# Optimization experiments

Hardware: AMD Instinct MI355X
Metric: run time of the kernel (lower is better)

The kernel has to match this reference:

```python
import math
import jax, jax.numpy as jnp
import numpy as np

HID = 8
QNUM = 22
NUM_A = 11
NUM_LAYER = 6


def _ln(x, g, b, eps=1e-5):
    m = jnp.mean(x, axis=-1, keepdims=True)
    v = jnp.mean((x - m) ** 2, axis=-1, keepdims=True)
    return (x - m) / jnp.sqrt(v + eps) * g + b


def _conv1d_s2(x, w):
    # x: [N, C, L], w: [O, I, K=2], stride 2, no padding, no bias
    return jax.lax.conv_general_dilated(x, w, (2,), 'VALID', dimension_numbers=('NCH', 'OIH', 'NCH'))


def _qembed(hf):
    # product state amplitudes of RY(hf_q)|0> per qubit: [cos(t/2), sin(t/2)], kron over qubits
    c = jnp.cos(hf / 2.0)
    s = jnp.sin(hf / 2.0)
    state = jnp.ones((1,), dtype=hf.dtype)
    for q in range(hf.shape[0]):
        state = jnp.kron(state, jnp.stack([c[q], s[q]]))
    return state  # [2^Q]


def setup_inputs() -> dict:
    key = jax.random.key(0)
    ks = jax.random.split(key, 32)
    ix_list = [2] * NUM_A  # 2 electrons per atom -> n_e = 22 (even, <= QNUM)
    pos_ix = np.concatenate([np.arange(n) for n in ix_list])
    atom_ix = np.concatenate([np.full(n, i) for i, n in enumerate(ix_list)])
    L = NUM_LAYER
    g = lambda i, shp, s=1.0: jax.random.normal(ks[i], shp, dtype=jnp.float32) * s
    return dict(
        pos_a=g(0, (NUM_A, 3), 3.0),
        ix_a=jnp.asarray(ix_list, dtype=jnp.int32),
        pos_ix=jnp.asarray(pos_ix, dtype=jnp.int32),
        atom_ix=jnp.asarray(atom_ix, dtype=jnp.int32),
        rpos_w=g(1, (10, 3), 1.0),
        emb_w=g(2, (HID, 4), 0.5),
        emb_b=jnp.zeros((HID,), jnp.float32),
        Wq=g(3, (L, HID, HID), 0.35), bq=jnp.zeros((L, HID), jnp.float32),
        Wk=g(4, (L, HID, HID), 0.35), bk=jnp.zeros((L, HID), jnp.float32),
        Wv=g(5, (L, HID, HID), 0.35), bv=jnp.zeros((L, HID), jnp.float32),
        Wo=g(6, (L, HID, HID), 0.35), bo=jnp.zeros((L, HID), jnp.float32),
        W1=g(7, (L, 4 * HID, HID), 0.35), b1=jnp.zeros((L, 4 * HID), jnp.float32),
        W2=g(8, (L, HID, 4 * HID), 0.18), b2=jnp.zeros((L, HID), jnp.float32),
        ln1_g=jnp.ones((L, HID), jnp.float32), ln1_b=jnp.zeros((L, HID), jnp.float32),
        ln2_g=jnp.ones((L, HID), jnp.float32), ln2_b=jnp.zeros((L, HID), jnp.float32),
        Wi=g(9, (2 * HID, HID), 0.35), bi=jnp.zeros((2 * HID,), jnp.float32),
        ni_g=jnp.ones((2 * HID,), jnp.float32), ni_b=jnp.zeros((2 * HID,), jnp.float32),
        conv_a_w=g(10, (2 * HID, 2 * HID, 2), 0.25),
        conv_e_w=g(11, (2 * HID, 2 * HID, 2), 0.25),
        Wout=g(12, (2 ** QNUM, 2 * HID), 0.05),
        bout=jnp.zeros((2 ** QNUM,), jnp.float32),
    )


def reference(pos_a, ix_a, pos_ix, atom_ix, rpos_w, emb_w, emb_b,
              Wq, bq, Wk, bk, Wv, bv, Wo, bo, W1, b1, W2, b2,
              ln1_g, ln1_b, ln2_g, ln2_b,
              Wi, bi, ni_g, ni_b, conv_a_w, conv_e_w, Wout, bout):
    n_e = pos_ix.shape[0]
    pos_e = rpos_w[pos_ix] + pos_a[atom_ix]                 # [n_e, 3]
    ae = pos_e[:, None, :] - pos_a[None, :, :]              # [n_e, A, 3]
    r_ae = jnp.linalg.norm(ae, axis=2, keepdims=True)       # [n_e, A, 1]
    seq = jnp.concatenate([ae, r_ae], axis=-1) @ emb_w.T + emb_b  # [n_e, A, HID]
    amp_proto = ix_a.astype(seq.dtype)[None, :, None]       # broadcast of expanded ix_a
    amp_ae = jnp.std(r_ae, ddof=1)
    bias_ae = jnp.mean(r_ae)
    scale = jnp.sqrt(jnp.asarray(HID, seq.dtype))
    for l in range(Wq.shape[0]):
        x = amp_proto * seq
        q = x @ Wq[l].T + bq[l]
        k = x @ Wk[l].T + bk[l]
        v = x @ Wv[l].T + bv[l]
        att = jax.nn.softmax(jnp.einsum('bqh,bkh->bqk', q, k) / scale, axis=-1)
        a = jnp.einsum('bqk,bkh->bqh', att, v) @ Wo[l].T + bo[l]
        x = _ln(x + a, ln1_g[l], ln1_b[l])
        f = jax.nn.relu(x @ W1[l].T + b1[l]) @ W2[l].T + b2[l]
        seq = _ln(x + f, ln2_g[l], ln2_b[l])
    # pseudo-inverse projection (detached in torch)
    ae_inv = jax.lax.stop_gradient(jnp.linalg.inv(emb_w.T @ emb_w) @ emb_w.T)  # [4, HID]
    r = jnp.einsum('h,bah->ba', ae_inv[-1], seq)[..., None]  # [n_e, A, 1]
    r = amp_ae * (r - jnp.mean(r)) / jnp.std(r, ddof=1) + bias_ae
    x = (jnp.exp(-r) * amp_proto * seq) @ Wi.T + bi          # [n_e, A, 2*HID]
    x = jnp.swapaxes(x, -2, -1)                              # [n_e, 2*HID, A]
    y = jnp.mean(x, axis=-1)                                 # [n_e, 2*HID]
    amp_r = jnp.mean(jnp.exp(-jnp.swapaxes(r, -2, -1)), axis=-1)  # [n_e, 1]
    pad = jnp.zeros((x.shape[0], x.shape[1], 1), x.dtype)
    n_iter_a = (x.shape[-1] + 1) // 2
    for _ in range(n_iter_a):
        x = _conv1d_s2(jnp.concatenate([x, pad], axis=-1), conv_a_w)
    x = (amp_r * _ln(y + x[..., 0], ni_g, ni_b)).T           # [2*HID, n_e]
    y = jnp.mean(x, axis=-1)                                 # [2*HID]
    amp_r2 = jnp.mean(amp_r.T, axis=-1)                      # [1]
    x = x[None]                                              # [1, 2*HID, n_e]
    pad = jnp.zeros((1, x.shape[1], 1), x.dtype)
    n_iter_e = (x.shape[-1] + 1) // 2
    for _ in range(n_iter_e):
        x = _conv1d_s2(jnp.concatenate([x, pad], axis=-1), conv_e_w)
    x = amp_r2 * _ln(y + x[0, :, 0], ni_g, ni_b)             # [2*HID]
    psi = x @ Wout.T + bout                                  # [2^QNUM]
    hf = jnp.asarray(([math.pi, 0.0] * (n_e // 2)) + [0.0] * (QNUM - n_e), dtype=psi.dtype)
    bos = _qembed(hf)
    return psi + bos * (2.0 ** (QNUM / 2))
```

## Files before the change

kernel.cpp:

```cpp
#include <hip/hip_runtime.h>
#include <math.h>

#define NE 22
#define NA 11
#define HD 8
#define H2 16
#define QN 22
#define NL 6
#define CPAD 12
#define CSTR 17

struct QCS { float c[QN]; float s[QN]; };

#define RL(v, l) __uint_as_float(__builtin_amdgcn_readlane(__float_as_uint(v), (l)))

__device__ __forceinline__ float block_reduce_sum(float v, float* red, int tid) {
  red[tid] = v;
  __syncthreads();
  for (int off = 128; off > 0; off >>= 1) {
    if (tid < off) red[tid] += red[tid + off];
    __syncthreads();
  }
  float s = red[0];
  __syncthreads();
  return s;
}

__device__ __forceinline__ void ln_vec(const float* x, int n, const float* __restrict__ g,
                                       const float* __restrict__ bb, float* o) {
  float m = 0.f;
  for (int i = 0; i < n; i++) m += x[i];
  m /= (float)n;
  float v = 0.f;
  for (int i = 0; i < n; i++) { float d = x[i] - m; v += d * d; }
  v /= (float)n;
  float is = 1.0f / sqrtf(v + 1e-5f);
  for (int i = 0; i < n; i++) o[i] = (x[i] - m) * is * g[i] + bb[i];
}

__global__ __launch_bounds__(256) void small_net_kernel(
    const float* __restrict__ pos_a, const int* __restrict__ ix_a,
    const int* __restrict__ pos_ix, const int* __restrict__ atom_ix,
    const float* __restrict__ rpos_w, const float* __restrict__ emb_w,
    const float* __restrict__ emb_b,
    const float* __restrict__ Wq, const float* __restrict__ bq,
    const float* __restrict__ Wk, const float* __restrict__ bk,
    const float* __restrict__ Wv, const float* __restrict__ bv,
    const float* __restrict__ Wo, const float* __restrict__ bo,
    const float* __restrict__ W1, const float* __restrict__ b1,
    const float* __restrict__ W2, const float* __restrict__ b2,
    const float* __restrict__ ln1_g, const float* __restrict__ ln1_b,
    const float* __restrict__ ln2_g, const float* __restrict__ ln2_b,
    const float* __restrict__ Wi, const float* __restrict__ bi,
    const float* __restrict__ ni_g, const float* __restrict__ ni_b,
    const float* __restrict__ conv_a_w, const float* __restrict__ conv_e_w,
    float* __restrict__ xf_out)
{
  const int tid = threadIdx.x;
  const int lane = tid & 63;
  const int b = tid / NA;
  const int a = tid % NA;
  const bool act = (tid < NE * NA);

  __shared__ __align__(16) float s_seq[NE][NA][HD];
  __shared__ __align__(16) float s_k[NE][NA][HD];
  __shared__ __align__(16) float s_v[NE][NA][HD];
  __shared__ float s_pos_e[NE][3];
  __shared__ float s_amp[NA];
  __shared__ float s_er[NE][NA];
  __shared__ float s_red[256];
  __shared__ float s_scal[8];
  __shared__ float s_aeinv[HD];
  __shared__ float convA[NE * CPAD * CSTR];
  __shared__ float convB[NE * CPAD * CSTR];
  __shared__ float s_y[NE][H2];
  __shared__ float s_ampr[NE];
  __shared__ float s_eA[24 * CSTR];
  __shared__ float s_eB[24 * CSTR];
  __shared__ float s_y2[H2];
  __shared__ float s_cewt[32 * H2];

  float cwr[8], wir[2];
  #pragma unroll
  for (int j = 0; j < 8; j++) cwr[j] = conv_a_w[j * 64 + lane];
  #pragma unroll
  for (int j = 0; j < 2; j++) wir[j] = Wi[j * 64 + lane];

  for (int s = tid; s < 512; s += 256) {
    int o = s >> 5, i = (s >> 1) & 15, k = s & 1;
    s_cewt[(i * 2 + k) * 16 + o] = conv_e_w[s];
  }

  if (tid < NE) {
    int p = pos_ix[tid], am = atom_ix[tid];
    for (int j = 0; j < 3; j++) s_pos_e[tid][j] = rpos_w[p * 3 + j] + pos_a[am * 3 + j];
  }
  if (tid < NA) s_amp[tid] = (float)ix_a[tid];
  __syncthreads();

  float rae = 0.f;
  if (act) {
    float d0 = s_pos_e[b][0] - pos_a[a * 3 + 0];
    float d1 = s_pos_e[b][1] - pos_a[a * 3 + 1];
    float d2 = s_pos_e[b][2] - pos_a[a * 3 + 2];
    rae = sqrtf(d0 * d0 + d1 * d1 + d2 * d2);
    float in4[4] = { d0, d1, d2, rae };
    #pragma unroll
    for (int h = 0; h < HD; h++) {
      float s = emb_b[h];
      #pragma unroll
      for (int j = 0; j < 4; j++) s += in4[j] * emb_w[h * 4 + j];
      s_seq[b][a][h] = s;
    }
  }
  {
    float sum = block_reduce_sum(act ? rae : 0.f, s_red, tid);
    float mean = sum / (float)(NE * NA);
    float d = act ? (rae - mean) : 0.f;
    float ss = block_reduce_sum(d * d, s_red, tid);
    if (tid == 0) { s_scal[0] = sqrtf(ss / (float)(NE * NA - 1)); s_scal[1] = mean; }
  }
  __syncthreads();

  const float iscale = 0.35355339059327373f;
  for (int l = 0; l < NL; l++) {
    float wr[12];
    wr[0] = Wq[l * 64 + lane];
    wr[1] = Wk[l * 64 + lane];
    wr[2] = Wv[l * 64 + lane];
    wr[3] = Wo[l * 64 + lane];
    #pragma unroll
    for (int j = 0; j < 4; j++) wr[4 + j] = W1[l * 256 + j * 64 + lane];
    #pragma unroll
    for (int j = 0; j < 4; j++) wr[8 + j] = W2[l * 256 + j * 64 + lane];

    float xv[HD], qq[HD];
    if (act) {
      float amp = s_amp[a];
      float4 sq0 = *(const float4*)&s_seq[b][a][0];
      float4 sq1 = *(const float4*)&s_seq[b][a][4];
      xv[0] = amp * sq0.x; xv[1] = amp * sq0.y; xv[2] = amp * sq0.z; xv[3] = amp * sq0.w;
      xv[4] = amp * sq1.x; xv[5] = amp * sq1.y; xv[6] = amp * sq1.z; xv[7] = amp * sq1.w;
      float kk[HD], vv[HD];
      #pragma unroll
      for (int h = 0; h < HD; h++) {
        float q_ = bq[l * HD + h], k_ = bk[l * HD + h], v_ = bv[l * HD + h];
        #pragma unroll
        for (int h2 = 0; h2 < HD; h2++) {
          q_ += xv[h2] * RL(wr[0], h * 8 + h2);
          k_ += xv[h2] * RL(wr[1], h * 8 + h2);
          v_ += xv[h2] * RL(wr[2], h * 8 + h2);
        }
        qq[h] = q_; kk[h] = k_; vv[h] = v_;
      }
      *(float4*)&s_k[b][a][0] = make_float4(kk[0], kk[1], kk[2], kk[3]);
      *(float4*)&s_k[b][a][4] = make_float4(kk[4], kk[5], kk[6], kk[7]);
      *(float4*)&s_v[b][a][0] = make_float4(vv[0], vv[1], vv[2], vv[3]);
      *(float4*)&s_v[b][a][4] = make_float4(vv[4], vv[5], vv[6], vv[7]);
    }
    __syncthreads();
    if (act) {
      float sc[NA];
      float mx = -1e30f;
      #pragma unroll
      for (int ka = 0; ka < NA; ka++) {
        float4 k0 = *(const float4*)&s_k[b][ka][0];
        float4 k1 = *(const float4*)&s_k[b][ka][4];
        float s = qq[0]*k0.x + qq[1]*k0.y + qq[2]*k0.z + qq[3]*k0.w
                + qq[4]*k1.x + qq[5]*k1.y + qq[6]*k1.z + qq[7]*k1.w;
        s *= iscale;
        sc[ka] = s;
        mx = fmaxf(mx, s);
      }
      float den = 0.f;
      #pragma unroll
      for (int ka = 0; ka < NA; ka++) { sc[ka] = expf(sc[ka] - mx); den += sc[ka]; }
      float inv_den = 1.0f / den;
      float av[HD];
      #pragma unroll
      for (int h = 0; h < HD; h++) av[h] = 0.f;
      #pragma unroll
      for (int ka = 0; ka < NA; ka++) {
        float4 v0 = *(const float4*)&s_v[b][ka][0];
        float4 v1 = *(const float4*)&s_v[b][ka][4];
        float p = sc[ka];
        av[0] += p * v0.x; av[1] += p * v0.y; av[2] += p * v0.z; av[3] += p * v0.w;
        av[4] += p * v1.x; av[5] += p * v1.y; av[6] += p * v1.z; av[7] += p * v1.w;
      }
      #pragma unroll
      for (int h = 0; h < HD; h++) av[h] *= inv_den;
      float xr[HD], xn[HD];
      #pragma unroll
      for (int h = 0; h < HD; h++) {
        float t = bo[l * HD + h];
        #pragma unroll
        for (int h2 = 0; h2 < HD; h2++) t += av[h2] * RL(wr[3], h * 8 + h2);
        xr[h] = xv[h] + t;
      }
      ln_vec(xr, HD, ln1_g + l * HD, ln1_b + l * HD, xn);
      float f2[HD];
      #pragma unroll
      for (int h = 0; h < HD; h++) f2[h] = b2[l * HD + h];
      #pragma unroll
      for (int o = 0; o < 32; o++) {
        float t = b1[l * 32 + o];
        #pragma unroll
        for (int h = 0; h < HD; h++) t += xn[h] * RL(wr[4 + ((o * 8 + h) >> 6)], (o * 8 + h) & 63);
        t = fmaxf(t, 0.f);
        #pragma unroll
        for (int h = 0; h < HD; h++) f2[h] += t * RL(wr[8 + ((h * 32 + o) >> 6)], (h * 32 + o) & 63);
      }
      #pragma unroll
      for (int h = 0; h < HD; h++) xr[h] = xn[h] + f2[h];
      ln_vec(xr, HD, ln2_g + l * HD, ln2_b + l * HD, xn);
      *(float4*)&s_seq[b][a][0] = make_float4(xn[0], xn[1], xn[2], xn[3]);
      *(float4*)&s_seq[b][a][4] = make_float4(xn[4], xn[5], xn[6], xn[7]);
    }
    __syncthreads();
  }

  if (tid == 0) {
    double M[4][8];
    for (int i = 0; i < 4; i++)
      for (int j = 0; j < 4; j++) {
        double s = 0.0;
        for (int h = 0; h < HD; h++) s += (double)emb_w[h * 4 + i] * (double)emb_w[h * 4 + j];
        M[i][j] = s;
        M[i][4 + j] = (i == j) ? 1.0 : 0.0;
      }
    for (int c = 0; c < 4; c++) {
      int piv = c;
      for (int r2 = c + 1; r2 < 4; r2++) if (fabs(M[r2][c]) > fabs(M[piv][c])) piv = r2;
      if (piv != c) for (int j = 0; j < 8; j++) { double t = M[c][j]; M[c][j] = M[piv][j]; M[piv][j] = t; }
      double dd = M[c][c];
      for (int j = 0; j < 8; j++) M[c][j] /= dd;
      for (int r2 = 0; r2 < 4; r2++) if (r2 != c) {
        double f = M[r2][c];
        for (int j = 0; j < 8; j++) M[r2][j] -= f * M[c][j];
      }
    }
    for (int h = 0; h < HD; h++) {
      double s = 0.0;
      for (int j = 0; j < 4; j++) s += M[3][4 + j] * (double)emb_w[h * 4 + j];
      s_aeinv[h] = (float)s;
    }
  }
  __syncthreads();

  float rv = 0.f;
  if (act) {
    #pragma unroll
    for (int h = 0; h < HD; h++) rv += s_aeinv[h] * s_seq[b][a][h];
  }
  {
    float sum = block_reduce_sum(act ? rv : 0.f, s_red, tid);
    float rm = sum / (float)(NE * NA);
    float d = act ? (rv - rm) : 0.f;
    float ss = block_reduce_sum(d * d, s_red, tid);
    float rs = sqrtf(ss / (float)(NE * NA - 1));
    if (act) {
      float rr = s_scal[0] * (rv - rm) / rs + s_scal[1];
      s_er[b][a] = expf(-rr);
    }
  }
  __syncthreads();

  if (act) {
    float e2 = s_er[b][a] * s_amp[a];
    float4 sq0 = *(const float4*)&s_seq[b][a][0];
    float4 sq1 = *(const float4*)&s_seq[b][a][4];
    float tv[HD] = { e2*sq0.x, e2*sq0.y, e2*sq0.z, e2*sq0.w,
                     e2*sq1.x, e2*sq1.y, e2*sq1.z, e2*sq1.w };
    #pragma unroll
    for (int o = 0; o < H2; o++) {
      float s = bi[o];
      #pragma unroll
      for (int h = 0; h < HD; h++) s += tv[h] * RL(wir[(o * 8 + h) >> 6], (o * 8 + h) & 63);
      convA[(b * CPAD + a) * CSTR + o] = s;
    }
  }
  for (int z = tid; z < NE * H2; z += 256)
    convA[((z >> 4) * CPAD + 11) * CSTR + (z & 15)] = 0.f;
  __syncthreads();

  for (int idx = tid; idx < NE * H2; idx += 256) {
    int bb = idx >> 4, o = idx & 15;
    float s = 0.f;
    for (int a2 = 0; a2 < NA; a2++) s += convA[(bb * CPAD + a2) * CSTR + o];
    s_y[bb][o] = s / (float)NA;
  }
  if (tid < NE) {
    float s = 0.f;
    for (int a2 = 0; a2 < NA; a2++) s += s_er[tid][a2];
    s_ampr[tid] = s / (float)NA;
  }
  __syncthreads();

  float* pin = convA;
  float* pout = convB;
  int L = NA;
  for (int it = 0; it < 6; it++) {
    int Lo = (L - 1) / 2 + 1;
    for (int pos = tid; pos < NE * Lo; pos += 256) {
      int bb = pos / Lo, j = pos - bb * Lo;
      const float* r0 = pin + (bb * CPAD + 2 * j) * CSTR;
      const float* r1 = r0 + CSTR;
      float x0[16], x1[16];
      #pragma unroll
      for (int i = 0; i < 16; i++) { x0[i] = r0[i]; x1[i] = r1[i]; }
      float* wrow = pout + (bb * CPAD + j) * CSTR;
      #pragma unroll
      for (int o = 0; o < 16; o++) {
        float acc = 0.f;
        #pragma unroll
        for (int i = 0; i < 16; i++) {
          acc += x0[i] * RL(cwr[((o * 16 + i) * 2) >> 6], ((o * 16 + i) * 2) & 63)
               + x1[i] * RL(cwr[((o * 16 + i) * 2 + 1) >> 6], ((o * 16 + i) * 2 + 1) & 63);
        }
        wrow[o] = acc;
      }
    }
    for (int z = tid; z < NE * H2; z += 256)
      pout[((z >> 4) * CPAD + Lo) * CSTR + (z & 15)] = 0.f;
    __syncthreads();
    float* t = pin; pin = pout; pout = t;
    L = Lo;
  }

  if (tid < NE) {
    float t[H2], oo[H2];
    #pragma unroll
    for (int o = 0; o < H2; o++) t[o] = s_y[tid][o] + pin[(tid * CPAD) * CSTR + o];
    ln_vec(t, H2, ni_g, ni_b, oo);
    float ar = s_ampr[tid];
    #pragma unroll
    for (int o = 0; o < H2; o++) s_eA[tid * CSTR + o] = ar * oo[o];
  }
  if (tid < H2) s_eA[NE * CSTR + tid] = 0.f;
  __syncthreads();
  if (tid < H2) {
    float s = 0.f;
    for (int bb = 0; bb < NE; bb++) s += s_eA[bb * CSTR + tid];
    s_y2[tid] = s / (float)NE;
  }
  if (tid == 0) {
    float s = 0.f;
    for (int bb = 0; bb < NE; bb++) s += s_ampr[bb];
    s_scal[4] = s / (float)NE;
  }
  __syncthreads();

  float* pinE = s_eA;
  float* poutE = s_eB;
  L = NE;
  for (int it = 0; it < 11; it++) {
    int Lo = (L - 1) / 2 + 1;
    for (int idx = tid; idx < Lo * H2; idx += 256) {
      int j = idx >> 4, o = idx & 15;
      const float* r0 = pinE + (2 * j) * CSTR;
      const float* r1 = r0 + CSTR;
      float acc = 0.f;
      #pragma unroll
      for (int i = 0; i < 16; i++)
        acc += r0[i] * s_cewt[(i * 2) * 16 + o] + r1[i] * s_cewt[(i * 2 + 1) * 16 + o];
      poutE[j * CSTR + o] = acc;
    }
    if (tid < H2) poutE[Lo * CSTR + tid] = 0.f;
    __syncthreads();
    float* t = pinE; pinE = poutE; poutE = t;
    L = Lo;
  }

  if (tid == 0) {
    float t[H2], oo[H2];
    for (int o = 0; o < H2; o++) t[o] = s_y2[o] + pinE[o];
    ln_vec(t, H2, ni_g, ni_b, oo);
    float a2 = s_scal[4];
    for (int o = 0; o < H2; o++) xf_out[o] = a2 * oo[o];
  }
}

__global__ __launch_bounds__(256) void psi_kernel(
    const float* __restrict__ Wout, const float* __restrict__ bout,
    const float* __restrict__ xf, float* __restrict__ out, QCS cs, int n)
{
  __shared__ float s_xf[H2];
  if (threadIdx.x < H2) s_xf[threadIdx.x] = xf[threadIdx.x];
  __syncthreads();
  int lane = threadIdx.x & 63;
  int waveBase = blockIdx.x * 256 + (threadIdx.x & ~63);
  if (waveBase >= n) return;
  const float4* W4 = (const float4*)Wout + (size_t)waveBase * 4;
  int q = lane & 3;
  float4 xq = make_float4(s_xf[q * 4], s_xf[q * 4 + 1], s_xf[q * 4 + 2], s_xf[q * 4 + 3]);
  #pragma unroll
  for (int j = 0; j < 4; j++) {
    float4 w = W4[j * 64 + lane];
    float p = w.x * xq.x + w.y * xq.y + w.z * xq.z + w.w * xq.w;
    p += __shfl_xor(p, 1, 64);
    p += __shfl_xor(p, 2, 64);
    if (q == 0) {
      int row = waveBase + j * 16 + (lane >> 2);
      float acc = bout[row] + p;
      unsigned int ii = (unsigned int)row;
      float pr = (float)(1 << (QN / 2));
      #pragma unroll
      for (int qb = 0; qb < QN; qb++)
        pr *= ((ii >> (QN - 1 - qb)) & 1u) ? cs.s[qb] : cs.c[qb];
      out[row] = acc + pr;
    }
  }
}

extern "C" void kernel_launch(void* const* d_in, const int* in_sizes, int n_in,
                              void* d_out, int out_size, void* d_ws, size_t ws_size,
                              hipStream_t stream) {
  const float* pos_a   = (const float*)d_in[0];
  const int*   ix_a    = (const int*)d_in[1];
  const int*   pos_ix  = (const int*)d_in[2];
  const int*   atom_ix = (const int*)d_in[3];
  const float* rpos_w  = (const float*)d_in[4];
  const float* emb_w   = (const float*)d_in[5];
  const float* emb_b   = (const float*)d_in[6];
  const float* Wq = (const float*)d_in[7];   const float* bq = (const float*)d_in[8];
  const float* Wk = (const float*)d_in[9];   const float* bk = (const float*)d_in[10];
  const float* Wv = (const float*)d_in[11];  const float* bv = (const float*)d_in[12];
  const float* Wo = (const float*)d_in[13];  const float* bo = (const float*)d_in[14];
  const float* W1 = (const float*)d_in[15];  const float* b1 = (const float*)d_in[16];
  const float* W2 = (const float*)d_in[17];  const float* b2 = (const float*)d_in[18];
  const float* ln1_g = (const float*)d_in[19]; const float* ln1_b = (const float*)d_in[20];
  const float* ln2_g = (const float*)d_in[21]; const float* ln2_b = (const float*)d_in[22];
  const float* Wi = (const float*)d_in[23];  const float* bi = (const float*)d_in[24];
  const float* ni_g = (const float*)d_in[25]; const float* ni_b = (const float*)d_in[26];
  const float* conv_a_w = (const float*)d_in[27];
  const float* conv_e_w = (const float*)d_in[28];
  const float* Wout = (const float*)d_in[29];
  const float* bout = (const float*)d_in[30];
  float* xf = (float*)d_ws;

  small_net_kernel<<<1, 256, 0, stream>>>(pos_a, ix_a, pos_ix, atom_ix, rpos_w,
      emb_w, emb_b, Wq, bq, Wk, bk, Wv, bv, Wo, bo, W1, b1, W2, b2,
      ln1_g, ln1_b, ln2_g, ln2_b, Wi, bi, ni_g, ni_b, conv_a_w, conv_e_w, xf);

  QCS cs;
  int n_e = in_sizes[2];
  for (int q = 0; q < QN; q++) {
    float hf = (q < n_e && (q % 2 == 0)) ? (float)M_PI : 0.0f;
    cs.c[q] = cosf(0.5f * hf);
    cs.s[q] = sinf(0.5f * hf);
  }

  int n = out_size;
  int blocks = (n + 255) / 256;
  psi_kernel<<<blocks, 256, 0, stream>>>(Wout, bout, xf, (float*)d_out, cs, n);
}
```

Before: 504.3 us.

## Split transformer layers into per-electron multi-block kernel before single-block tail

Moves the six attention/MLP layers out of the single 256-thread block into a separate kernel with one 128-thread block per electron. Within each block a thread computes one (atom, hidden) element, and the block exchanges data through shared memory. Sequence and distance results go to workspace for a separate tail kernel that does the reductions and convolutions. The aim is to cut the serial per-thread work on the long single-block critical path by spreading it across many CUs. The cost is an extra kernel launch, a global-memory round trip, and many more block barriers per layer.

```diff
diff --git a/kernel.cpp b/kernel.cpp
--- a/kernel.cpp
+++ b/kernel.cpp
@@ -38,7 +38,7 @@
   for (int i = 0; i < n; i++) o[i] = (x[i] - m) * is * g[i] + bb[i];
 }
 
-__global__ __launch_bounds__(256) void small_net_kernel(
+__global__ __launch_bounds__(128, 1) void layers_kernel(
     const float* __restrict__ pos_a, const int* __restrict__ ix_a,
     const int* __restrict__ pos_ix, const int* __restrict__ atom_ix,
     const float* __restrict__ rpos_w, const float* __restrict__ emb_w,
@@ -51,9 +51,210 @@
     const float* __restrict__ W2, const float* __restrict__ b2,
     const float* __restrict__ ln1_g, const float* __restrict__ ln1_b,
     const float* __restrict__ ln2_g, const float* __restrict__ ln2_b,
+    float* __restrict__ seq_out, float* __restrict__ rae_out)
+{
+  const int e = blockIdx.x;
+  const int tid = threadIdx.x;
+  const int a = tid >> 3;
+  const int h = tid & 7;
+  const bool act = (a < NA);
+
+  __shared__ __align__(16) float sseq[NA][HD];
+  __shared__ __align__(16) float sx[NA][HD];
+  __shared__ __align__(16) float sq_[NA][HD];
+  __shared__ __align__(16) float sk_[NA][HD];
+  __shared__ __align__(16) float sv_[NA][HD];
+  __shared__ __align__(16) float sav[NA][HD];
+  __shared__ float ss[NA][12];
+  __shared__ __align__(16) float sh_[NA][32];
+
+  float amp_a = 0.f;
+  if (act) {
+    amp_a = (float)ix_a[a];
+    int p = pos_ix[e], am = atom_ix[e];
+    float d0 = rpos_w[p*3+0] + pos_a[am*3+0] - pos_a[a*3+0];
+    float d1 = rpos_w[p*3+1] + pos_a[am*3+1] - pos_a[a*3+1];
+    float d2 = rpos_w[p*3+2] + pos_a[am*3+2] - pos_a[a*3+2];
+    float rae = sqrtf(d0*d0 + d1*d1 + d2*d2);
+    float s = emb_b[h] + d0*emb_w[h*4+0] + d1*emb_w[h*4+1]
+            + d2*emb_w[h*4+2] + rae*emb_w[h*4+3];
+    sseq[a][h] = s;
+    if (h == 0) rae_out[e*NA + a] = rae;
+  }
+  __syncthreads();
+
+  const float iscale = 0.35355339059327373f;
+  for (int l = 0; l < NL; l++) {
+    float wq[8], wk[8], wv[8], wo[8], w1v[4][8], w2v[32];
+    {
+      const float4* q4 = (const float4*)(Wq + l*64 + h*8);
+      float4 t0 = q4[0], t1 = q4[1];
+      wq[0]=t0.x; wq[1]=t0.y; wq[2]=t0.z; wq[3]=t0.w; wq[4]=t1.x; wq[5]=t1.y; wq[6]=t1.z; wq[7]=t1.w;
+      const float4* k4 = (const float4*)(Wk + l*64 + h*8);
+      t0 = k4[0]; t1 = k4[1];
+      wk[0]=t0.x; wk[1]=t0.y; wk[2]=t0.z; wk[3]=t0.w; wk[4]=t1.x; wk[5]=t1.y; wk[6]=t1.z; wk[7]=t1.w;
+      const float4* v4 = (const float4*)(Wv + l*64 + h*8);
+      t0 = v4[0]; t1 = v4[1];
+      wv[0]=t0.x; wv[1]=t0.y; wv[2]=t0.z; wv[3]=t0.w; wv[4]=t1.x; wv[5]=t1.y; wv[6]=t1.z; wv[7]=t1.w;
+      const float4* o4 = (const float4*)(Wo + l*64 + h*8);
+      t0 = o4[0]; t1 = o4[1];
+      wo[0]=t0.x; wo[1]=t0.y; wo[2]=t0.z; wo[3]=t0.w; wo[4]=t1.x; wo[5]=t1.y; wo[6]=t1.z; wo[7]=t1.w;
+      #pragma unroll
+      for (int j = 0; j < 4; j++) {
+        const float4* w14 = (const float4*)(W1 + l*256 + (j*8 + h)*8);
+        float4 u0 = w14[0], u1 = w14[1];
+        w1v[j][0]=u0.x; w1v[j][1]=u0.y; w1v[j][2]=u0.z; w1v[j][3]=u0.w;
+        w1v[j][4]=u1.x; w1v[j][5]=u1.y; w1v[j][6]=u1.z; w1v[j][7]=u1.w;
+      }
+      const float4* w24 = (const float4*)(W2 + l*256 + h*32);
+      #pragma unroll
+      for (int j = 0; j < 8; j++) {
+        float4 u = w24[j];
+        w2v[j*4+0]=u.x; w2v[j*4+1]=u.y; w2v[j*4+2]=u.z; w2v[j*4+3]=u.w;
+      }
+    }
+    float bqv = bq[l*8+h], bkv = bk[l*8+h], bvv = bv[l*8+h], bov = bo[l*8+h];
+    float b1v[4];
+    #pragma unroll
+    for (int j = 0; j < 4; j++) b1v[j] = b1[l*32 + j*8 + h];
+    float b2v = b2[l*8+h];
+    float g1 = ln1_g[l*8+h], be1 = ln1_b[l*8+h];
+    float g2 = ln2_g[l*8+h], be2 = ln2_b[l*8+h];
+
+    float xah = 0.f;
+    if (act) { xah = amp_a * sseq[a][h]; sx[a][h] = xah; }
+    __syncthreads();
+
+    if (act) {
+      float xr[8];
+      float4 r0 = *(const float4*)&sx[a][0];
+      float4 r1 = *(const float4*)&sx[a][4];
+      xr[0]=r0.x; xr[1]=r0.y; xr[2]=r0.z; xr[3]=r0.w; xr[4]=r1.x; xr[5]=r1.y; xr[6]=r1.z; xr[7]=r1.w;
+      float q_ = bqv, k_ = bkv, v_ = bvv;
+      #pragma unroll
+      for (int h2 = 0; h2 < 8; h2++) {
+        q_ += xr[h2]*wq[h2];
+        k_ += xr[h2]*wk[h2];
+        v_ += xr[h2]*wv[h2];
+      }
+      sq_[a][h] = q_; sk_[a][h] = k_; sv_[a][h] = v_;
+    }
+    __syncthreads();
+
+    if (act) {
+      float4 q0 = *(const float4*)&sq_[a][0];
+      float4 q1 = *(const float4*)&sq_[a][4];
+      {
+        int ka = h;
+        float4 k0 = *(const float4*)&sk_[ka][0];
+        float4 k1 = *(const float4*)&sk_[ka][4];
+        ss[a][ka] = iscale * (q0.x*k0.x + q0.y*k0.y + q0.z*k0.z + q0.w*k0.w
+                            + q1.x*k1.x + q1.y*k1.y + q1.z*k1.z + q1.w*k1.w);
+      }
+      if (h < 3) {
+        int ka = 8 + h;
+        float4 k0 = *(const float4*)&sk_[ka][0];
+        float4 k1 = *(const float4*)&sk_[ka][4];
+        ss[a][ka] = iscale * (q0.x*k0.x + q0.y*k0.y + q0.z*k0.z + q0.w*k0.w
+                            + q1.x*k1.x + q1.y*k1.y + q1.z*k1.z + q1.w*k1.w);
+      }
+    }
+    __syncthreads();
+
+    float avh = 0.f;
+    if (act) {
+      float sc[NA], mx = -1e30f;
+      #pragma unroll
+      for (int ka = 0; ka < NA; ka++) { sc[ka] = ss[a][ka]; mx = fmaxf(mx, sc[ka]); }
+      float den = 0.f;
+      #pragma unroll
+      for (int ka = 0; ka < NA; ka++) { sc[ka] = expf(sc[ka] - mx); den += sc[ka]; }
+      float inv_den = 1.0f / den;
+      #pragma unroll
+      for (int ka = 0; ka < NA; ka++) avh += sc[ka] * sv_[ka][h];
+      avh *= inv_den;
+      sav[a][h] = avh;
+    }
+    __syncthreads();
+
+    if (act) {
+      float av[8];
+      float4 r0 = *(const float4*)&sav[a][0];
+      float4 r1 = *(const float4*)&sav[a][4];
+      av[0]=r0.x; av[1]=r0.y; av[2]=r0.z; av[3]=r0.w; av[4]=r1.x; av[5]=r1.y; av[6]=r1.z; av[7]=r1.w;
+      float t = bov;
+      #pragma unroll
+      for (int h2 = 0; h2 < 8; h2++) t += av[h2]*wo[h2];
+      sq_[a][h] = xah + t;
+    }
+    __syncthreads();
+
+    float xnh = 0.f;
+    if (act) {
+      float4 r0 = *(const float4*)&sq_[a][0];
+      float4 r1 = *(const float4*)&sq_[a][4];
+      float m = (r0.x+r0.y+r0.z+r0.w+r1.x+r1.y+r1.z+r1.w) * 0.125f;
+      float d, v = 0.f;
+      d=r0.x-m; v+=d*d; d=r0.y-m; v+=d*d; d=r0.z-m; v+=d*d; d=r0.w-m; v+=d*d;
+      d=r1.x-m; v+=d*d; d=r1.y-m; v+=d*d; d=r1.z-m; v+=d*d; d=r1.w-m; v+=d*d;
+      v *= 0.125f;
+      float is = 1.0f / sqrtf(v + 1e-5f);
+      float own = (h<4) ? (&r0.x)[h] : (&r1.x)[h-4];
+      xnh = (own - m) * is * g1 + be1;
+      sk_[a][h] = xnh;
+    }
+    __syncthreads();
+
+    if (act) {
+      float xn[8];
+      float4 r0 = *(const float4*)&sk_[a][0];
+      float4 r1 = *(const float4*)&sk_[a][4];
+      xn[0]=r0.x; xn[1]=r0.y; xn[2]=r0.z; xn[3]=r0.w; xn[4]=r1.x; xn[5]=r1.y; xn[6]=r1.z; xn[7]=r1.w;
+      #pragma unroll
+      for (int j = 0; j < 4; j++) {
+        float t = b1v[j];
+        #pragma unroll
+        for (int h2 = 0; h2 < 8; h2++) t += xn[h2]*w1v[j][h2];
+        sh_[a][j*8+h] = fmaxf(t, 0.f);
+      }
+    }
+    __syncthreads();
+
+    if (act) {
+      float f2 = b2v;
+      #pragma unroll
+      for (int j = 0; j < 8; j++) {
+        float4 hv = *(const float4*)&sh_[a][j*4];
+        f2 += hv.x*w2v[j*4+0] + hv.y*w2v[j*4+1] + hv.z*w2v[j*4+2] + hv.w*w2v[j*4+3];
+      }
+      sq_[a][h] = xnh + f2;
+    }
+    __syncthreads();
+
+    if (act) {
+      float4 r0 = *(const float4*)&sq_[a][0];
+      float4 r1 = *(const float4*)&sq_[a][4];
+      float m = (r0.x+r0.y+r0.z+r0.w+r1.x+r1.y+r1.z+r1.w) * 0.125f;
+      float d, v = 0.f;
+      d=r0.x-m; v+=d*d; d=r0.y-m; v+=d*d; d=r0.z-m; v+=d*d; d=r0.w-m; v+=d*d;
+      d=r1.x-m; v+=d*d; d=r1.y-m; v+=d*d; d=r1.z-m; v+=d*d; d=r1.w-m; v+=d*d;
+      v *= 0.125f;
+      float is = 1.0f / sqrtf(v + 1e-5f);
+      float own = (h<4) ? (&r0.x)[h] : (&r1.x)[h-4];
+      sseq[a][h] = (own - m) * is * g2 + be2;
+    }
+    __syncthreads();
+  }
+
+  if (act) seq_out[e*NA*HD + a*HD + h] = sseq[a][h];
+}
+
+__global__ __launch_bounds__(256) void tail_kernel(
+    const int* __restrict__ ix_a, const float* __restrict__ emb_w,
     const float* __restrict__ Wi, const float* __restrict__ bi,
     const float* __restrict__ ni_g, const float* __restrict__ ni_b,
     const float* __restrict__ conv_a_w, const float* __restrict__ conv_e_w,
+    const float* __restrict__ seq_ws, const float* __restrict__ rae_ws,
     float* __restrict__ xf_out)
 {
   const int tid = threadIdx.x;
@@ -63,9 +264,6 @@
   const bool act = (tid < NE * NA);
 
   __shared__ __align__(16) float s_seq[NE][NA][HD];
-  __shared__ __align__(16) float s_k[NE][NA][HD];
-  __shared__ __align__(16) float s_v[NE][NA][HD];
-  __shared__ float s_pos_e[NE][3];
   __shared__ float s_amp[NA];
   __shared__ float s_er[NE][NA];
   __shared__ float s_red[256];
@@ -90,29 +288,12 @@
     int o = s >> 5, i = (s >> 1) & 15, k = s & 1;
     s_cewt[(i * 2 + k) * 16 + o] = conv_e_w[s];
   }
-
-  if (tid < NE) {
-    int p = pos_ix[tid], am = atom_ix[tid];
-    for (int j = 0; j < 3; j++) s_pos_e[tid][j] = rpos_w[p * 3 + j] + pos_a[am * 3 + j];
-  }
+  for (int i = tid; i < NE*NA*HD/4; i += 256)
+    ((float4*)s_seq)[i] = ((const float4*)seq_ws)[i];
   if (tid < NA) s_amp[tid] = (float)ix_a[tid];
-  __syncthreads();
-
-  float rae = 0.f;
-  if (act) {
-    float d0 = s_pos_e[b][0] - pos_a[a * 3 + 0];
-    float d1 = s_pos_e[b][1] - pos_a[a * 3 + 1];
-    float d2 = s_pos_e[b][2] - pos_a[a * 3 + 2];
-    rae = sqrtf(d0 * d0 + d1 * d1 + d2 * d2);
-    float in4[4] = { d0, d1, d2, rae };
-    #pragma unroll
-    for (int h = 0; h < HD; h++) {
-      float s = emb_b[h];
-      #pragma unroll
-      for (int j = 0; j < 4; j++) s += in4[j] * emb_w[h * 4 + j];
-      s_seq[b][a][h] = s;
-    }
-  }
+  float rae = act ? rae_ws[tid] : 0.f;
+  __syncthreads();
+
   {
     float sum = block_reduce_sum(act ? rae : 0.f, s_red, tid);
     float mean = sum / (float)(NE * NA);
@@ -121,103 +302,6 @@
     if (tid == 0) { s_scal[0] = sqrtf(ss / (float)(NE * NA - 1)); s_scal[1] = mean; }
   }
   __syncthreads();
-
-  const float iscale = 0.35355339059327373f;
-  for (int l = 0; l < NL; l++) {
-    float wr[12];
-    wr[0] = Wq[l * 64 + lane];
-    wr[1] = Wk[l * 64 + lane];
-    wr[2] = Wv[l * 64 + lane];
-    wr[3] = Wo[l * 64 + lane];
-    #pragma unroll
-    for (int j = 0; j < 4; j++) wr[4 + j] = W1[l * 256 + j * 64 + lane];
-    #pragma unroll
-    for (int j = 0; j < 4; j++) wr[8 + j] = W2[l * 256 + j * 64 + lane];
-
-    float xv[HD], qq[HD];
-    if (act) {
-      float amp = s_amp[a];
-      float4 sq0 = *(const float4*)&s_seq[b][a][0];
-      float4 sq1 = *(const float4*)&s_seq[b][a][4];
-      xv[0] = amp * sq0.x; xv[1] = amp * sq0.y; xv[2] = amp * sq0.z; xv[3] = amp * sq0.w;
-      xv[4] = amp * sq1.x; xv[5] = amp * sq1.y; xv[6] = amp * sq1.z; xv[7] = amp * sq1.w;
-      float kk[HD], vv[HD];
-      #pragma unroll
-      for (int h = 0; h < HD; h++) {
-        float q_ = bq[l * HD + h], k_ = bk[l * HD + h], v_ = bv[l * HD + h];
-        #pragma unroll
-        for (int h2 = 0; h2 < HD; h2++) {
-          q_ += xv[h2] * RL(wr[0], h * 8 + h2);
-          k_ += xv[h2] * RL(wr[1], h * 8 + h2);
-          v_ += xv[h2] * RL(wr[2], h * 8 + h2);
-        }
-        qq[h] = q_; kk[h] = k_; vv[h] = v_;
-      }
-      *(float4*)&s_k[b][a][0] = make_float4(kk[0], kk[1], kk[2], kk[3]);
-      *(float4*)&s_k[b][a][4] = make_float4(kk[4], kk[5], kk[6], kk[7]);
-      *(float4*)&s_v[b][a][0] = make_float4(vv[0], vv[1], vv[2], vv[3]);
-      *(float4*)&s_v[b][a][4] = make_float4(vv[4], vv[5], vv[6], vv[7]);
-    }
-    __syncthreads();
-    if (act) {
-      float sc[NA];
-      float mx = -1e30f;
-      #pragma unroll
-      for (int ka = 0; ka < NA; ka++) {
-        float4 k0 = *(const float4*)&s_k[b][ka][0];
-        float4 k1 = *(const float4*)&s_k[b][ka][4];
-        float s = qq[0]*k0.x + qq[1]*k0.y + qq[2]*k0.z + qq[3]*k0.w
-                + qq[4]*k1.x + qq[5]*k1.y + qq[6]*k1.z + qq[7]*k1.w;
-        s *= iscale;
-        sc[ka] = s;
-        mx = fmaxf(mx, s);
-      }
-      float den = 0.f;
-      #pragma unroll
-      for (int ka = 0; ka < NA; ka++) { sc[ka] = expf(sc[ka] - mx); den += sc[ka]; }
-      float inv_den = 1.0f / den;
-      float av[HD];
-      #pragma unroll
-      for (int h = 0; h < HD; h++) av[h] = 0.f;
-      #pragma unroll
-      for (int ka = 0; ka < NA; ka++) {
-        float4 v0 = *(const float4*)&s_v[b][ka][0];
-        float4 v1 = *(const float4*)&s_v[b][ka][4];
-        float p = sc[ka];
-        av[0] += p * v0.x; av[1] += p * v0.y; av[2] += p * v0.z; av[3] += p * v0.w;
-        av[4] += p * v1.x; av[5] += p * v1.y; av[6] += p * v1.z; av[7] += p * v1.w;
-      }
-      #pragma unroll
-      for (int h = 0; h < HD; h++) av[h] *= inv_den;
-      float xr[HD], xn[HD];
-      #pragma unroll
-      for (int h = 0; h < HD; h++) {
-        float t = bo[l * HD + h];
-        #pragma unroll
-        for (int h2 = 0; h2 < HD; h2++) t += av[h2] * RL(wr[3], h * 8 + h2);
-        xr[h] = xv[h] + t;
-      }
-      ln_vec(xr, HD, ln1_g + l * HD, ln1_b + l * HD, xn);
-      float f2[HD];
-      #pragma unroll
-      for (int h = 0; h < HD; h++) f2[h] = b2[l * HD + h];
-      #pragma unroll
-      for (int o = 0; o < 32; o++) {
-        float t = b1[l * 32 + o];
-        #pragma unroll
-        for (int h = 0; h < HD; h++) t += xn[h] * RL(wr[4 + ((o * 8 + h) >> 6)], (o * 8 + h) & 63);
-        t = fmaxf(t, 0.f);
-        #pragma unroll
-        for (int h = 0; h < HD; h++) f2[h] += t * RL(wr[8 + ((h * 32 + o) >> 6)], (h * 32 + o) & 63);
-      }
-      #pragma unroll
-      for (int h = 0; h < HD; h++) xr[h] = xn[h] + f2[h];
-      ln_vec(xr, HD, ln2_g + l * HD, ln2_b + l * HD, xn);
-      *(float4*)&s_seq[b][a][0] = make_float4(xn[0], xn[1], xn[2], xn[3]);
-      *(float4*)&s_seq[b][a][4] = make_float4(xn[4], xn[5], xn[6], xn[7]);
-    }
-    __syncthreads();
-  }
 
   if (tid == 0) {
     double M[4][8];
@@ -436,11 +520,18 @@
   const float* conv_e_w = (const float*)d_in[28];
   const float* Wout = (const float*)d_in[29];
   const float* bout = (const float*)d_in[30];
-  float* xf = (float*)d_ws;
-
-  small_net_kernel<<<1, 256, 0, stream>>>(pos_a, ix_a, pos_ix, atom_ix, rpos_w,
+
+  float* ws = (float*)d_ws;
+  float* xf      = ws;
+  float* seq_ws  = ws + 64;
+  float* rae_ws  = ws + 64 + NE*NA*HD;
+
+  layers_kernel<<<NE, 128, 0, stream>>>(pos_a, ix_a, pos_ix, atom_ix, rpos_w,
       emb_w, emb_b, Wq, bq, Wk, bk, Wv, bv, Wo, bo, W1, b1, W2, b2,
-      ln1_g, ln1_b, ln2_g, ln2_b, Wi, bi, ni_g, ni_b, conv_a_w, conv_e_w, xf);
+      ln1_g, ln1_b, ln2_g, ln2_b, seq_ws, rae_ws);
+
+  tail_kernel<<<1, 256, 0, stream>>>(ix_a, emb_w, Wi, bi, ni_g, ni_b,
+      conv_a_w, conv_e_w, seq_ws, rae_ws, xf);
 
   QCS cs;
   int n_e = in_sizes[2];
```

Result: faster. 483.6 us (-4.1%).
